# Optimization experiments

Hardware: AMD Instinct MI355X
Metric: run time of the kernel (lower is better)

The kernel has to match this reference:

```python
import jax, jax.numpy as jnp
import numpy as np

N_RAYS = 32768
N_OBJ = 16
N_SAMPLES = 32   # n_pts_object
N_BASE = 64      # pre-existing coarse samples per ray
MISS = 1e10      # sentinel for non-intersecting slots (sorts to the end)


def _make_transforms(key):
    """Random rigid+scale world-to-object transforms, pytorch3d row-vector convention:
    p' = p @ M[:3,:3] + M[3,:3]."""
    k1, k2, k3 = jax.random.split(key, 3)
    A = jax.random.normal(k1, (N_OBJ, 3, 3))
    Q, _ = jnp.linalg.qr(A)                                   # orthonormal 3x3
    t = jax.random.normal(k2, (N_OBJ, 3)) * 5.0               # translations
    s = jax.random.uniform(k3, (N_OBJ, 3), minval=0.5, maxval=2.0)
    eye = jnp.tile(jnp.eye(4, dtype=jnp.float32), (N_OBJ, 1, 1))
    rots = eye.at[:, :3, :3].set(Q.astype(jnp.float32))
    trafos = rots.at[:, 3, :3].set(t)
    scales = eye.at[:, 0, 0].set(s[:, 0]).at[:, 1, 1].set(s[:, 1]).at[:, 2, 2].set(s[:, 2])
    return trafos, rots, scales


def setup_inputs() -> dict:
    key = jax.random.key(0)
    k0, k1, k2, k3 = jax.random.split(key, 4)
    origins = jax.random.normal(k0, (N_RAYS, 3), dtype=jnp.float32) * 2.0
    directions = jax.random.normal(k1, (N_RAYS, 3), dtype=jnp.float32)
    lengths = jnp.sort(jax.random.uniform(k2, (N_RAYS, N_BASE), dtype=jnp.float32,
                                          minval=0.1, maxval=20.0), axis=-1)
    trafos, rots, scales = _make_transforms(k3)
    return {"origins": origins, "directions": directions, "lengths": lengths,
            "trafos_w2o": trafos, "rots_w2o": rots, "scales_w2o": scales}


def reference(origins, directions, lengths, trafos_w2o, rots_w2o, scales_w2o):
    N = origins.shape[0]
    M = trafos_w2o.shape[0]
    S = N_SAMPLES

    d_w = directions / jnp.linalg.norm(directions, axis=-1, keepdims=True)

    # compose transforms (row-vector convention: compose(m1, m2) -> m1 @ m2)
    pt_mat = trafos_w2o @ scales_w2o     # points world->object, [M,4,4]
    dir_mat = rots_w2o @ scales_w2o      # directions world->object

    # rays in each object frame: [M,N,3]
    origins_o = jnp.einsum('ni,mij->mnj', origins, pt_mat[:, :3, :3]) + pt_mat[:, None, 3, :3]
    dirs_o = jnp.einsum('ni,mij->mnj', d_w, dir_mat[:, :3, :3])
    dirs_o = dirs_o / jnp.linalg.norm(dirs_o, axis=-1, keepdims=True)

    # slab ray-AABB intersection against unit box [-1,1]^3
    inv = 1.0 / dirs_o
    t0 = (-1.0 - origins_o) * inv
    t1 = (1.0 - origins_o) * inv
    tmin = jnp.max(jnp.minimum(t0, t1), axis=-1)   # [M,N]
    tmax = jnp.min(jnp.maximum(t0, t1), axis=-1)
    hit = (tmax > tmin) & (tmax > 0.0)
    t_in = jnp.maximum(tmin, 0.0)

    # BoxRaysampler: linspace between entry and exit
    lin = jnp.linspace(0.0, 1.0, S, dtype=origins.dtype)
    z_o = t_in[..., None] + (tmax - t_in)[..., None] * lin          # [M,N,S]

    # object-space sample points / dirs
    pts_o = origins_o[:, :, None] + dirs_o[:, :, None] * z_o[..., None]   # [M,N,S,3]
    dirs_o_s = jnp.broadcast_to(dirs_o[:, :, None], pts_o.shape)

    # back to world -> z along world ray
    o2w = jnp.linalg.inv(pt_mat)
    pts_w = jnp.einsum('mnsi,mij->mnsj', pts_o, o2w[:, :3, :3]) + o2w[:, None, None, 3, :3]
    z_w = jnp.einsum('mnsj,nj->mns', pts_w - origins[None, :, None], d_w)
    z_w = jnp.where(hit[..., None], z_w, MISS)                      # mask misses

    # scatter into per-ray lengths (static worst-case size), then sort per ray
    z_flat = jnp.transpose(z_w, (1, 0, 2)).reshape(N, M * S)        # [N, M*S]
    lengths_new = jnp.concatenate([lengths, z_flat], axis=-1)       # [N, B+M*S]

    node_ids = jnp.broadcast_to(jnp.arange(M, dtype=jnp.int32)[:, None, None], (M, N, S))
    node_ids = jnp.where(hit[..., None], node_ids, -1)
    node_flat = jnp.concatenate(
        [jnp.full((N, lengths.shape[-1]), -1, dtype=jnp.int32),
         jnp.transpose(node_ids, (1, 0, 2)).reshape(N, M * S)], axis=-1)
    mask_flat = jnp.concatenate(
        [jnp.zeros((N, lengths.shape[-1]), dtype=bool),
         jnp.transpose(jnp.broadcast_to(hit[..., None], (M, N, S)), (1, 0, 2)).reshape(N, M * S)],
        axis=-1)

    order = jnp.argsort(lengths_new, axis=-1)
    sorted_lengths = jnp.take_along_axis(lengths_new, order, axis=-1)
    sorted_nodes = jnp.take_along_axis(node_flat, order, axis=-1)
    sorted_mask = jnp.take_along_axis(mask_flat, order, axis=-1)

    # flattened object-space samples (zeroed for misses; static shape)
    pts_flat = (pts_o * hit[..., None, None]).reshape(-1, 3)
    dirs_flat = (dirs_o_s * hit[..., None, None]).reshape(-1, 3)

    return sorted_lengths, sorted_nodes, sorted_mask, pts_flat, dirs_flat
```

## Files before the change

### kernel.cpp

```cpp
#include <hip/hip_runtime.h>

#define NR    32768
#define NOBJ  16
#define NS    32
#define NB    64
#define WIDTH 576
#define MISSV 1e10f

__device__ __forceinline__ float fmulr(float a, float b){ return __fmul_rn(a,b); }
__device__ __forceinline__ float faddr(float a, float b){ return __fadd_rn(a,b); }
__device__ __forceinline__ float fsubr(float a, float b){ return __fsub_rn(a,b); }
__device__ __forceinline__ float fdvr (float a, float b){ return __fdiv_rn(a,b); }

struct RayObj {
  float oo[3];
  float dd[3];
  float t_in, dt;
  float dn;
  bool  hit;
};

__device__ __forceinline__ void ray_obj_setup(
    const float* __restrict__ origins, const float* __restrict__ dirs,
    const float* __restrict__ trafos,  const float* __restrict__ scales,
    int m, int n, RayObj& R)
{
  const float o0 = origins[3*n+0], o1 = origins[3*n+1], o2 = origins[3*n+2];
  const float r0 = dirs[3*n+0],    r1 = dirs[3*n+1],    r2 = dirs[3*n+2];
  const float nn = __fsqrt_rn(faddr(faddr(fmulr(r0,r0), fmulr(r1,r1)), fmulr(r2,r2)));
  const float w0 = fdvr(r0,nn), w1 = fdvr(r1,nn), w2 = fdvr(r2,nn);

  const float* T = trafos + 16*m;
  const float* S = scales + 16*m;
  const float s0 = S[0], s1 = S[5], s2 = S[10];
  const float pm00 = fmulr(T[0],  s0), pm01 = fmulr(T[1],  s1), pm02 = fmulr(T[2],  s2);
  const float pm10 = fmulr(T[4],  s0), pm11 = fmulr(T[5],  s1), pm12 = fmulr(T[6],  s2);
  const float pm20 = fmulr(T[8],  s0), pm21 = fmulr(T[9],  s1), pm22 = fmulr(T[10], s2);
  const float tm0  = fmulr(T[12], s0), tm1  = fmulr(T[13], s1), tm2  = fmulr(T[14], s2);

  const float oo0 = faddr(faddr(faddr(fmulr(o0,pm00), fmulr(o1,pm10)), fmulr(o2,pm20)), tm0);
  const float oo1 = faddr(faddr(faddr(fmulr(o0,pm01), fmulr(o1,pm11)), fmulr(o2,pm21)), tm1);
  const float oo2 = faddr(faddr(faddr(fmulr(o0,pm02), fmulr(o1,pm12)), fmulr(o2,pm22)), tm2);
  const float du0 = faddr(faddr(fmulr(w0,pm00), fmulr(w1,pm10)), fmulr(w2,pm20));
  const float du1 = faddr(faddr(fmulr(w0,pm01), fmulr(w1,pm11)), fmulr(w2,pm21));
  const float du2 = faddr(faddr(fmulr(w0,pm02), fmulr(w1,pm12)), fmulr(w2,pm22));
  const float dn  = __fsqrt_rn(faddr(faddr(fmulr(du0,du0), fmulr(du1,du1)), fmulr(du2,du2)));
  const float dd0 = fdvr(du0,dn), dd1 = fdvr(du1,dn), dd2 = fdvr(du2,dn);

  const float i0 = fdvr(1.0f, dd0), i1 = fdvr(1.0f, dd1), i2 = fdvr(1.0f, dd2);
  const float a0 = fmulr(fsubr(-1.0f, oo0), i0), b0 = fmulr(fsubr(1.0f, oo0), i0);
  const float a1 = fmulr(fsubr(-1.0f, oo1), i1), b1 = fmulr(fsubr(1.0f, oo1), i1);
  const float a2 = fmulr(fsubr(-1.0f, oo2), i2), b2 = fmulr(fsubr(1.0f, oo2), i2);
  const float tmn = fmaxf(fmaxf(fminf(a0,b0), fminf(a1,b1)), fminf(a2,b2));
  const float tmx = fminf(fminf(fmaxf(a0,b0), fmaxf(a1,b1)), fmaxf(a2,b2));

  R.hit  = (tmx > tmn) && (tmx > 0.0f);
  R.t_in = fmaxf(tmn, 0.0f);
  R.dt   = fsubr(tmx, R.t_in);
  R.dn   = dn;
  R.oo[0]=oo0; R.oo[1]=oo1; R.oo[2]=oo2;
  R.dd[0]=dd0; R.dd[1]=dd1; R.dd[2]=dd2;
}

__device__ __forceinline__ int count_run_reg(float A2, float B2, float IB2,
                                             float key, bool tie)
{
  if (B2 <= 0.0f) {
    return (A2 < key || (A2 == key && tie)) ? NS : 0;
  }
  float g = floorf(fmulr(fsubr(key, A2), IB2));
  g = fminf(33.0f, fmaxf(-1.0f, g));
  int c = (int)g + 1;
  c = c < 0 ? 0 : (c > NS ? NS : c);
  while (c > 0) {
    const float v = faddr(A2, fmulr(B2, (float)(c-1)));
    if (v < key || (v == key && tie)) break;
    --c;
  }
  while (c < NS) {
    const float v = faddr(A2, fmulr(B2, (float)c));
    if (v < key || (v == key && tie)) ++c; else break;
  }
  return c;
}

struct PtsS  { float ld[64][8]; };
struct SortS {
  float sBase[4][NB];
  float sA[4][NOBJ], sB[4][NOBJ], sIB[4][NOBJ];
  float sL[4][WIDTH], sN[4][WIDTH];
};
union __align__(16) Smem { PtsS p; SortS s; };

__global__ __launch_bounds__(256) void k_fused(
    const float* __restrict__ origins, const float* __restrict__ dirs,
    const float* __restrict__ lengths,
    const float* __restrict__ trafos,  const float* __restrict__ scales,
    float* __restrict__ outL, float* __restrict__ outN, float* __restrict__ outM,
    float* __restrict__ outP, float* __restrict__ outD)
{
  __shared__ Smem U;
  const int tid  = threadIdx.x;
  const int role = blockIdx.x & 1;
  const int bid  = blockIdx.x >> 1;

  if (role == 0) {
    const int m   = bid >> 9;
    const int n0  = (bid & 511) << 6;
    if (tid < 64) {
      RayObj R;
      ray_obj_setup(origins, dirs, trafos, scales, m, n0 + tid, R);
      const bool h = R.hit;
      U.p.ld[tid][0] = h ? R.oo[0] : 0.0f;
      U.p.ld[tid][1] = h ? R.oo[1] : 0.0f;
      U.p.ld[tid][2] = h ? R.oo[2] : 0.0f;
      U.p.ld[tid][3] = h ? R.dd[0] : 0.0f;
      U.p.ld[tid][4] = h ? R.dd[1] : 0.0f;
      U.p.ld[tid][5] = h ? R.t_in  : 0.0f;
      U.p.ld[tid][6] = h ? R.dt    : 0.0f;
      U.p.ld[tid][7] = h ? R.dd[2] : 0.0f;
    }
    __syncthreads();
    const size_t base = (size_t)(m * NR + n0) * 96;
    float4* P4 = (float4*)(outP + base);
    float4* D4 = (float4*)(outD + base);
    #pragma unroll
    for (int it = 0; it < 6; ++it) {
      const int f   = tid + (it << 8);
      const int rr  = f / 24;
      const int off = (f - rr * 24) * 4;
      const float oox = U.p.ld[rr][0], ooy = U.p.ld[rr][1], ooz = U.p.ld[rr][2];
      const float ddx = U.p.ld[rr][3], ddy = U.p.ld[rr][4], ddz = U.p.ld[rr][7];
      const float ti  = U.p.ld[rr][5], dtt = U.p.ld[rr][6];
      float4 p, d;
      float* pp = (float*)&p; float* dv = (float*)&d;
      #pragma unroll
      for (int i = 0; i < 4; ++i) {
        const int idx = off + i;
        const int s   = idx / 3;
        const int c   = idx - s * 3;
        const float z  = ti + dtt * ((float)s * (1.0f/31.0f));
        const float oc = (c == 0) ? oox : ((c == 1) ? ooy : ooz);
        const float dc = (c == 0) ? ddx : ((c == 1) ? ddy : ddz);
        pp[i] = oc + dc * z;
        dv[i] = dc;
      }
      P4[f] = p;
      D4[f] = d;
    }
    return;
  }

  const int wv   = tid >> 6;
  const int lane = tid & 63;
  const int n    = bid * 4 + wv;

  bool myhit = false;
  if (lane < NOBJ) {
    RayObj R;
    ray_obj_setup(origins, dirs, trafos, scales, lane, n, R);
    myhit = R.hit;
    float myA = MISSV, myB = -1.0f, myIB = 0.0f;
    if (R.hit) {
      const double invdn = 1.0 / (double)R.dn;
      myA = (float)((double)R.t_in * invdn);
      myB = (float)(((double)R.dt * invdn) * (1.0 / 31.0));
      if (!(myB > 0.0f)) myB = 0.0f;
      myIB = (myB > 0.0f) ? (1.0f / myB) : 0.0f;
    }
    U.s.sA[wv][lane]  = myA;
    U.s.sB[wv][lane]  = R.hit ? myB : -1.0f;
    U.s.sIB[wv][lane] = myIB;
  }
  const unsigned hm = (unsigned)(__ballot(myhit) & 0xFFFFull);
  const int H = __popc(hm);
  asm volatile("" ::: "memory");

  float kr[9];
  kr[0] = lengths[n * NB + lane];
  U.s.sBase[wv][lane] = kr[0];
  #pragma unroll
  for (int k = 1; k < 9; ++k) {
    const int m0 = 2*(k-1) + (lane >> 5);
    const int s  = lane & 31;
    if ((hm >> m0) & 1u) {
      const float A_ = U.s.sA[wv][m0], B_ = U.s.sB[wv][m0];
      kr[k] = faddr(A_, fmulr(B_, (float)s));
    } else {
      kr[k] = MISSV;
    }
  }
  asm volatile("" ::: "memory");

  const float* K = U.s.sBase[wv];
  int rnk[9];
  rnk[0] = lane;
  #pragma unroll
  for (int k = 1; k < 9; ++k) {
    const int m = 2*(k-1) + (lane >> 5);
    const int s = lane & 31;
    if ((hm >> m) & 1u) {
      int c = 0;
      const float key = kr[k];
      #pragma unroll
      for (int st = 64; st >= 1; st >>= 1) {
        const int t2 = c + st;
        if (t2 <= NB && K[t2-1] <= key) c = t2;
      }
      rnk[k] = s + c;
    } else {
      const int MB = __popc((~hm) & ((1u << m) - 1u) & 0xFFFFu);
      rnk[k] = NB + NS*H + NS*MB + s;
    }
  }

  unsigned mm = hm;
  while (mm) {
    const int m2 = __ffs(mm) - 1; mm &= mm - 1;
    const float A2  = U.s.sA[wv][m2];
    const float B2  = U.s.sB[wv][m2];
    const float IB2 = U.s.sIB[wv][m2];
    rnk[0] += count_run_reg(A2, B2, IB2, kr[0], false);
    #pragma unroll
    for (int k = 1; k < 9; ++k) {
      const int m = 2*(k-1) + (lane >> 5);
      if (((hm >> m) & 1u) && m != m2)
        rnk[k] += count_run_reg(A2, B2, IB2, kr[k], m2 < m);
    }
  }

  U.s.sL[wv][rnk[0]] = kr[0];
  U.s.sN[wv][rnk[0]] = -1.0f;
  #pragma unroll
  for (int k = 1; k < 9; ++k) {
    const int m = 2*(k-1) + (lane >> 5);
    const bool h = (hm >> m) & 1u;
    U.s.sL[wv][rnk[k]] = kr[k];
    U.s.sN[wv][rnk[k]] = h ? (float)m : -1.0f;
  }
  asm volatile("" ::: "memory");

  float4* pL = (float4*)(outL + (size_t)n * WIDTH);
  float4* pN = (float4*)(outN + (size_t)n * WIDTH);
  float4* pM = (float4*)(outM + (size_t)n * WIDTH);
  const float4* qL = (const float4*)U.s.sL[wv];
  const float4* qN = (const float4*)U.s.sN[wv];
  for (int i = lane; i < WIDTH/4; i += 64) pL[i] = qL[i];
  for (int i = lane; i < WIDTH/4; i += 64) {
    const float4 nv = qN[i];
    float4 mv;
    mv.x = nv.x >= 0.0f ? 1.0f : 0.0f;
    mv.y = nv.y >= 0.0f ? 1.0f : 0.0f;
    mv.z = nv.z >= 0.0f ? 1.0f : 0.0f;
    mv.w = nv.w >= 0.0f ? 1.0f : 0.0f;
    pN[i] = nv;
    pM[i] = mv;
  }
}

extern "C" void kernel_launch(void* const* d_in, const int* in_sizes, int n_in,
                              void* d_out, int out_size, void* d_ws, size_t ws_size,
                              hipStream_t stream)
{
  (void)in_sizes; (void)n_in; (void)out_size; (void)d_ws; (void)ws_size;
  const float* origins = (const float*)d_in[0];
  const float* dirs    = (const float*)d_in[1];
  const float* lengths = (const float*)d_in[2];
  const float* trafos  = (const float*)d_in[3];
  const float* scales  = (const float*)d_in[5];

  float* out  = (float*)d_out;
  float* outL = out;
  float* outN = out + (size_t)NR * WIDTH;
  float* outM = out + (size_t)2 * NR * WIDTH;
  float* outP = out + (size_t)3 * NR * WIDTH;
  float* outD = outP + (size_t)NOBJ * NR * NS * 3;

  hipLaunchKernelGGL(k_fused, dim3(16384), dim3(256), 0, stream,
                     origins, dirs, lengths, trafos, scales,
                     outL, outN, outM, outP, outD);
}
```

Before: 622.7 us.

## Unify point and sort roles per ray, reuse ray setup, use nontemporal stores

Before, half the blocks computed per-object sample points and the other half did the per-ray sort, so ray-object setup ran twice. Now each wavefront handles one ray: it runs setup once for 16 objects, writes the object-space points and directions, then does the sort. All output writes become nontemporal vector stores and launch bounds ask for 4 blocks per CU. The trade-off is that point stores are now scattered across object rows (24 float4 per object per ray) rather than long contiguous runs per block.

```diff
diff --git a/kernel.cpp b/kernel.cpp
--- a/kernel.cpp
+++ b/kernel.cpp
@@ -6,6 +6,8 @@
 #define NB    64
 #define WIDTH 576
 #define MISSV 1e10f
+
+typedef float f32x4 __attribute__((ext_vector_type(4)));
 
 __device__ __forceinline__ float fmulr(float a, float b){ return __fmul_rn(a,b); }
 __device__ __forceinline__ float faddr(float a, float b){ return __fadd_rn(a,b); }
@@ -84,56 +86,68 @@
   return c;
 }
 
-struct PtsS  { float ld[64][8]; };
-struct SortS {
+struct __align__(16) SortS {
+  float sOD[4][NOBJ][8];
   float sBase[4][NB];
   float sA[4][NOBJ], sB[4][NOBJ], sIB[4][NOBJ];
   float sL[4][WIDTH], sN[4][WIDTH];
 };
-union __align__(16) Smem { PtsS p; SortS s; };
-
-__global__ __launch_bounds__(256) void k_fused(
+
+__global__ __launch_bounds__(256, 4) void k_unified(
     const float* __restrict__ origins, const float* __restrict__ dirs,
     const float* __restrict__ lengths,
     const float* __restrict__ trafos,  const float* __restrict__ scales,
     float* __restrict__ outL, float* __restrict__ outN, float* __restrict__ outM,
     float* __restrict__ outP, float* __restrict__ outD)
 {
-  __shared__ Smem U;
+  __shared__ SortS U;
   const int tid  = threadIdx.x;
-  const int role = blockIdx.x & 1;
-  const int bid  = blockIdx.x >> 1;
-
-  if (role == 0) {
-    const int m   = bid >> 9;
-    const int n0  = (bid & 511) << 6;
-    if (tid < 64) {
-      RayObj R;
-      ray_obj_setup(origins, dirs, trafos, scales, m, n0 + tid, R);
-      const bool h = R.hit;
-      U.p.ld[tid][0] = h ? R.oo[0] : 0.0f;
-      U.p.ld[tid][1] = h ? R.oo[1] : 0.0f;
-      U.p.ld[tid][2] = h ? R.oo[2] : 0.0f;
-      U.p.ld[tid][3] = h ? R.dd[0] : 0.0f;
-      U.p.ld[tid][4] = h ? R.dd[1] : 0.0f;
-      U.p.ld[tid][5] = h ? R.t_in  : 0.0f;
-      U.p.ld[tid][6] = h ? R.dt    : 0.0f;
-      U.p.ld[tid][7] = h ? R.dd[2] : 0.0f;
-    }
-    __syncthreads();
-    const size_t base = (size_t)(m * NR + n0) * 96;
-    float4* P4 = (float4*)(outP + base);
-    float4* D4 = (float4*)(outD + base);
+  const int wv   = tid >> 6;
+  const int lane = tid & 63;
+  const int n    = blockIdx.x * 4 + wv;
+
+  bool myhit = false;
+  if (lane < NOBJ) {
+    RayObj R;
+    ray_obj_setup(origins, dirs, trafos, scales, lane, n, R);
+    myhit = R.hit;
+    const bool h = R.hit;
+    U.sOD[wv][lane][0] = h ? R.oo[0] : 0.0f;
+    U.sOD[wv][lane][1] = h ? R.oo[1] : 0.0f;
+    U.sOD[wv][lane][2] = h ? R.oo[2] : 0.0f;
+    U.sOD[wv][lane][3] = h ? R.dd[0] : 0.0f;
+    U.sOD[wv][lane][4] = h ? R.dd[1] : 0.0f;
+    U.sOD[wv][lane][5] = h ? R.t_in  : 0.0f;
+    U.sOD[wv][lane][6] = h ? R.dt    : 0.0f;
+    U.sOD[wv][lane][7] = h ? R.dd[2] : 0.0f;
+
+    float myA = MISSV, myB = -1.0f, myIB = 0.0f;
+    if (R.hit) {
+      const double invdn = 1.0 / (double)R.dn;
+      myA = (float)((double)R.t_in * invdn);
+      myB = (float)(((double)R.dt * invdn) * (1.0 / 31.0));
+      if (!(myB > 0.0f)) myB = 0.0f;
+      myIB = (myB > 0.0f) ? (1.0f / myB) : 0.0f;
+    }
+    U.sA[wv][lane]  = myA;
+    U.sB[wv][lane]  = R.hit ? myB : -1.0f;
+    U.sIB[wv][lane] = myIB;
+  }
+  const unsigned hm = (unsigned)(__ballot(myhit) & 0xFFFFull);
+  const int H = __popc(hm);
+  asm volatile("" ::: "memory");
+
+  {
     #pragma unroll
     for (int it = 0; it < 6; ++it) {
-      const int f   = tid + (it << 8);
-      const int rr  = f / 24;
-      const int off = (f - rr * 24) * 4;
-      const float oox = U.p.ld[rr][0], ooy = U.p.ld[rr][1], ooz = U.p.ld[rr][2];
-      const float ddx = U.p.ld[rr][3], ddy = U.p.ld[rr][4], ddz = U.p.ld[rr][7];
-      const float ti  = U.p.ld[rr][5], dtt = U.p.ld[rr][6];
-      float4 p, d;
-      float* pp = (float*)&p; float* dv = (float*)&d;
+      const int f   = it * 64 + lane;
+      const int mo  = f / 24;
+      const int w4  = f - mo * 24;
+      const int off = w4 * 4;
+      const float oox = U.sOD[wv][mo][0], ooy = U.sOD[wv][mo][1], ooz = U.sOD[wv][mo][2];
+      const float ddx = U.sOD[wv][mo][3], ddy = U.sOD[wv][mo][4], ddz = U.sOD[wv][mo][7];
+      const float ti  = U.sOD[wv][mo][5], dtt = U.sOD[wv][mo][6];
+      f32x4 p, d;
       #pragma unroll
       for (int i = 0; i < 4; ++i) {
         const int idx = off + i;
@@ -142,49 +156,24 @@
         const float z  = ti + dtt * ((float)s * (1.0f/31.0f));
         const float oc = (c == 0) ? oox : ((c == 1) ? ooy : ooz);
         const float dc = (c == 0) ? ddx : ((c == 1) ? ddy : ddz);
-        pp[i] = oc + dc * z;
-        dv[i] = dc;
+        p[i] = oc + dc * z;
+        d[i] = dc;
       }
-      P4[f] = p;
-      D4[f] = d;
-    }
-    return;
-  }
-
-  const int wv   = tid >> 6;
-  const int lane = tid & 63;
-  const int n    = bid * 4 + wv;
-
-  bool myhit = false;
-  if (lane < NOBJ) {
-    RayObj R;
-    ray_obj_setup(origins, dirs, trafos, scales, lane, n, R);
-    myhit = R.hit;
-    float myA = MISSV, myB = -1.0f, myIB = 0.0f;
-    if (R.hit) {
-      const double invdn = 1.0 / (double)R.dn;
-      myA = (float)((double)R.t_in * invdn);
-      myB = (float)(((double)R.dt * invdn) * (1.0 / 31.0));
-      if (!(myB > 0.0f)) myB = 0.0f;
-      myIB = (myB > 0.0f) ? (1.0f / myB) : 0.0f;
-    }
-    U.s.sA[wv][lane]  = myA;
-    U.s.sB[wv][lane]  = R.hit ? myB : -1.0f;
-    U.s.sIB[wv][lane] = myIB;
-  }
-  const unsigned hm = (unsigned)(__ballot(myhit) & 0xFFFFull);
-  const int H = __popc(hm);
-  asm volatile("" ::: "memory");
+      const size_t base4 = ((size_t)mo * NR + n) * 24;
+      __builtin_nontemporal_store(p, (f32x4*)outP + base4 + w4);
+      __builtin_nontemporal_store(d, (f32x4*)outD + base4 + w4);
+    }
+  }
 
   float kr[9];
   kr[0] = lengths[n * NB + lane];
-  U.s.sBase[wv][lane] = kr[0];
+  U.sBase[wv][lane] = kr[0];
   #pragma unroll
   for (int k = 1; k < 9; ++k) {
     const int m0 = 2*(k-1) + (lane >> 5);
     const int s  = lane & 31;
     if ((hm >> m0) & 1u) {
-      const float A_ = U.s.sA[wv][m0], B_ = U.s.sB[wv][m0];
+      const float A_ = U.sA[wv][m0], B_ = U.sB[wv][m0];
       kr[k] = faddr(A_, fmulr(B_, (float)s));
     } else {
       kr[k] = MISSV;
@@ -192,7 +181,7 @@
   }
   asm volatile("" ::: "memory");
 
-  const float* K = U.s.sBase[wv];
+  const float* K = U.sBase[wv];
   int rnk[9];
   rnk[0] = lane;
   #pragma unroll
@@ -217,9 +206,9 @@
   unsigned mm = hm;
   while (mm) {
     const int m2 = __ffs(mm) - 1; mm &= mm - 1;
-    const float A2  = U.s.sA[wv][m2];
-    const float B2  = U.s.sB[wv][m2];
-    const float IB2 = U.s.sIB[wv][m2];
+    const float A2  = U.sA[wv][m2];
+    const float B2  = U.sB[wv][m2];
+    const float IB2 = U.sIB[wv][m2];
     rnk[0] += count_run_reg(A2, B2, IB2, kr[0], false);
     #pragma unroll
     for (int k = 1; k < 9; ++k) {
@@ -229,32 +218,33 @@
     }
   }
 
-  U.s.sL[wv][rnk[0]] = kr[0];
-  U.s.sN[wv][rnk[0]] = -1.0f;
+  U.sL[wv][rnk[0]] = kr[0];
+  U.sN[wv][rnk[0]] = -1.0f;
   #pragma unroll
   for (int k = 1; k < 9; ++k) {
     const int m = 2*(k-1) + (lane >> 5);
     const bool h = (hm >> m) & 1u;
-    U.s.sL[wv][rnk[k]] = kr[k];
-    U.s.sN[wv][rnk[k]] = h ? (float)m : -1.0f;
+    U.sL[wv][rnk[k]] = kr[k];
+    U.sN[wv][rnk[k]] = h ? (float)m : -1.0f;
   }
   asm volatile("" ::: "memory");
 
-  float4* pL = (float4*)(outL + (size_t)n * WIDTH);
-  float4* pN = (float4*)(outN + (size_t)n * WIDTH);
-  float4* pM = (float4*)(outM + (size_t)n * WIDTH);
-  const float4* qL = (const float4*)U.s.sL[wv];
-  const float4* qN = (const float4*)U.s.sN[wv];
-  for (int i = lane; i < WIDTH/4; i += 64) pL[i] = qL[i];
+  f32x4* pL = (f32x4*)(outL + (size_t)n * WIDTH);
+  f32x4* pN = (f32x4*)(outN + (size_t)n * WIDTH);
+  f32x4* pM = (f32x4*)(outM + (size_t)n * WIDTH);
+  const f32x4* qL = (const f32x4*)U.sL[wv];
+  const f32x4* qN = (const f32x4*)U.sN[wv];
+  for (int i = lane; i < WIDTH/4; i += 64)
+    __builtin_nontemporal_store(qL[i], pL + i);
   for (int i = lane; i < WIDTH/4; i += 64) {
-    const float4 nv = qN[i];
-    float4 mv;
-    mv.x = nv.x >= 0.0f ? 1.0f : 0.0f;
-    mv.y = nv.y >= 0.0f ? 1.0f : 0.0f;
-    mv.z = nv.z >= 0.0f ? 1.0f : 0.0f;
-    mv.w = nv.w >= 0.0f ? 1.0f : 0.0f;
-    pN[i] = nv;
-    pM[i] = mv;
+    const f32x4 nv = qN[i];
+    f32x4 mv;
+    mv[0] = nv[0] >= 0.0f ? 1.0f : 0.0f;
+    mv[1] = nv[1] >= 0.0f ? 1.0f : 0.0f;
+    mv[2] = nv[2] >= 0.0f ? 1.0f : 0.0f;
+    mv[3] = nv[3] >= 0.0f ? 1.0f : 0.0f;
+    __builtin_nontemporal_store(nv, pN + i);
+    __builtin_nontemporal_store(mv, pM + i);
   }
 }
 
@@ -276,7 +266,7 @@
   float* outP = out + (size_t)3 * NR * WIDTH;
   float* outD = outP + (size_t)NOBJ * NR * NS * 3;
 
-  hipLaunchKernelGGL(k_fused, dim3(16384), dim3(256), 0, stream,
+  hipLaunchKernelGGL(k_unified, dim3(NR/4), dim3(256), 0, stream,
                      origins, dirs, lengths, trafos, scales,
                      outL, outN, outM, outP, outD);
 }
```

Measured after the change: 630.3 us. No clear change (+1.2%).
